# Performance work log

Hardware: AMD Instinct MI355X
Metric: run time of the kernel (lower is better)

Reference implementation:

```python
import jax, jax.numpy as jnp
import numpy as np

GRID = 10
C_IN = 4          # input_dim // (grid*grid) = 400 // 100
HID = 128         # lstm hidden_dim
NV = 6            # num_vehicles
PH = 10           # pred_horizon
BN_EPS = 1e-5


def setup_inputs() -> dict:
    key = jax.random.key(0)
    ks = jax.random.split(key, 20)
    def n(k, shape, scale=0.05):
        return jax.random.normal(k, shape, jnp.float32) * scale
    return {
        "observations": jax.random.normal(ks[0], (1024, 32, 400), jnp.float32),
        # CNN
        "conv1_w": n(ks[1], (16, C_IN, 3, 3)), "conv1_b": n(ks[2], (16,)),
        "conv2_w": n(ks[3], (32, 16, 3, 3)), "conv2_b": n(ks[4], (32,)),
        # FCN (BatchNorm in eval mode: running stats + affine)
        "fc1_w": n(ks[5], (128, 128)), "fc1_b": n(ks[6], (128,)),
        "bn1_gamma": jnp.ones((128,), jnp.float32), "bn1_beta": jnp.zeros((128,), jnp.float32),
        "bn1_mean": jnp.zeros((128,), jnp.float32), "bn1_var": jnp.ones((128,), jnp.float32),
        "fc2_w": n(ks[7], (64, 128)), "fc2_b": n(ks[8], (64,)),
        "bn2_gamma": jnp.ones((64,), jnp.float32), "bn2_beta": jnp.zeros((64,), jnp.float32),
        "bn2_mean": jnp.zeros((64,), jnp.float32), "bn2_var": jnp.ones((64,), jnp.float32),
        # encoder LSTM (torch gate order i,f,g,o; b = b_ih + b_hh fused)
        "enc_w_ih": n(ks[9], (4 * HID, 64)), "enc_w_hh": n(ks[10], (4 * HID, HID)),
        "enc_b": n(ks[11], (4 * HID,)),
        # decoder LSTM
        "dec_w_ih": n(ks[12], (4 * HID, HID)), "dec_w_hh": n(ks[13], (4 * HID, HID)),
        "dec_b": n(ks[14], (4 * HID,)),
        # output head
        "out_w": n(ks[15], (2 * NV, HID)), "out_b": n(ks[16], (2 * NV,)),
    }


def _conv(x, w, b):
    y = jax.lax.conv_general_dilated(x, w, (1, 1), "SAME",
                                     dimension_numbers=("NCHW", "OIHW", "NCHW"))
    return y + b[None, :, None, None]


def _maxpool2(x):
    # MaxPool2d(2,2) with floor (drops odd trailing row/col) == VALID
    return jax.lax.reduce_window(x, -jnp.inf, jax.lax.max, (1, 1, 2, 2), (1, 1, 2, 2), "VALID")


def _bn(x, g, b, m, v):
    return (x - m) * jax.lax.rsqrt(v + BN_EPS) * g + b


def _lstm_cell(x, h, c, w_ih, w_hh, b):
    gates = x @ w_ih.T + h @ w_hh.T + b
    i, f, g, o = jnp.split(gates, 4, axis=-1)
    c_new = jax.nn.sigmoid(f) * c + jax.nn.sigmoid(i) * jnp.tanh(g)
    h_new = jax.nn.sigmoid(o) * jnp.tanh(c_new)
    return h_new, c_new


def reference(observations, conv1_w, conv1_b, conv2_w, conv2_b,
              fc1_w, fc1_b, bn1_gamma, bn1_beta, bn1_mean, bn1_var,
              fc2_w, fc2_b, bn2_gamma, bn2_beta, bn2_mean, bn2_var,
              enc_w_ih, enc_w_hh, enc_b, dec_w_ih, dec_w_hh, dec_b,
              out_w, out_b):
    B, T, D = observations.shape
    # ---- fuse the per-frame Python loop: batch all B*T frames at once ----
    x = observations.reshape(B * T, C_IN, GRID, GRID)
    x = _maxpool2(jax.nn.relu(_conv(x, conv1_w, conv1_b)))   # [BT,16,5,5]
    x = _maxpool2(jax.nn.relu(_conv(x, conv2_w, conv2_b)))   # [BT,32,2,2]
    x = x.reshape(B * T, -1)                                 # [BT,128]
    x = jax.nn.relu(_bn(x @ fc1_w.T + fc1_b, bn1_gamma, bn1_beta, bn1_mean, bn1_var))
    x = jax.nn.relu(_bn(x @ fc2_w.T + fc2_b, bn2_gamma, bn2_beta, bn2_mean, bn2_var))
    feats = x.reshape(B, T, 64)

    # ---- encoder LSTM ----
    h0 = jnp.zeros((B, HID), feats.dtype)
    c0 = jnp.zeros((B, HID), feats.dtype)
    def enc_step(carry, xt):
        h, c = carry
        h, c = _lstm_cell(xt, h, c, enc_w_ih, enc_w_hh, enc_b)
        return (h, c), h
    (h_n, c_n), hs = jax.lax.scan(enc_step, (h0, c0), jnp.swapaxes(feats, 0, 1))
    dec_x = hs[-1]  # encoder_output[:, -1]

    def dec_step(carry, _):
        x_in, h, c = carry
        h, c = _lstm_cell(x_in, h, c, dec_w_ih, dec_w_hh, dec_b)
        pred = h @ out_w.T + out_b
        return (h, h, c), pred
    _, preds = jax.lax.scan(dec_step, (dec_x, h_n, c_n), None, length=PH)
    return jnp.swapaxes(preds, 0, 1)  # [B, PH, 2*NV]
```

## Files before the change

### kernel.cpp

```cpp
#include <hip/hip_runtime.h>
#include <hip/hip_bf16.h>
#include <hip/hip_fp16.h>

constexpr int GT = 32768;
constexpr int TSEQ = 32;

typedef _Float16 h2 __attribute__((ext_vector_type(2)));

#if defined(__has_builtin)
#if __has_builtin(__builtin_amdgcn_fdot2)
#define FDOT2(a, b, c) __builtin_amdgcn_fdot2((a), (b), (c), false)
#endif
#endif
#ifndef FDOT2
#define FDOT2(a, b, c) fmaf((float)(a).x, (float)(b).x, fmaf((float)(a).y, (float)(b).y, (c)))
#endif

__device__ __forceinline__ h2 pack2(float a, float b) {
  h2 v; v.x = (_Float16)a; v.y = (_Float16)b; return v;
}

constexpr size_t OBS_T  = 0;
constexpr size_t POOL1H = 13107200;
constexpr size_t POOL2H = 0;
constexpr size_t Y1H    = 2097152;
constexpr size_t FEATSH = 19660800;
constexpr size_t GX     = 0;
constexpr size_t WB     = 26214400;
constexpr size_t W_C1   = WB + 0;
constexpr size_t W_C2H  = WB + 576;
constexpr size_t W_F1H  = WB + 2880;
constexpr size_t B_F1   = WB + 11072;
constexpr size_t W_F2H  = WB + 11200;
constexpr size_t B_F2   = WB + 15296;
constexpr size_t W_ENCXH= WB + 15360;
constexpr size_t W_ENCHH= WB + 31744;
constexpr size_t B_ENC  = WB + 64512;
constexpr size_t W_DECH = WB + 65024;
constexpr size_t B_DEC  = WB + 97792;

__device__ __forceinline__ float sigf(float x)  { return 1.f / (1.f + __expf(-x)); }
__device__ __forceinline__ float tanhfast(float x) { return 1.f - 2.f / (__expf(2.f * x) + 1.f); }

__global__ __launch_bounds__(256) void k_setup(
    const float* __restrict__ c1w, const float* __restrict__ c2w,
    const float* __restrict__ f1w, const float* __restrict__ f1b,
    const float* __restrict__ g1, const float* __restrict__ be1,
    const float* __restrict__ m1, const float* __restrict__ v1,
    const float* __restrict__ f2w, const float* __restrict__ f2b,
    const float* __restrict__ g2, const float* __restrict__ be2,
    const float* __restrict__ m2, const float* __restrict__ v2,
    const float* __restrict__ ewih, const float* __restrict__ ewhh, const float* __restrict__ eb,
    const float* __restrict__ dwih, const float* __restrict__ dwhh, const float* __restrict__ db,
    float* __restrict__ ws) {
  h2* wsh = (h2*)ws;
  long i = (long)blockIdx.x * 256 + threadIdx.x;
  if (i < 576)  { int c = i & 15, r = i >> 4; ws[W_C1 + i] = c1w[c * 36 + r]; return; }
  i -= 576;
  if (i < 2304) { int co = i & 31, q = i >> 5; int ci2 = q / 9, t9 = q % 9;
    wsh[W_C2H + i] = pack2(c2w[co * 144 + (2 * ci2) * 9 + t9],
                           c2w[co * 144 + (2 * ci2 + 1) * 9 + t9]); return; }
  i -= 2304;
  if (i < 8192) { int j = i & 127, q = i >> 7; int co2 = q >> 2, pos = q & 3;
    float s = g1[j] * rsqrtf(v1[j] + 1e-5f);
    wsh[W_F1H + i] = pack2(f1w[j * 128 + 8 * co2 + pos] * s,
                           f1w[j * 128 + 8 * co2 + 4 + pos] * s); return; }
  i -= 8192;
  if (i < 128) { int j = i; float s = g1[j] * rsqrtf(v1[j] + 1e-5f);
    ws[B_F1 + i] = (f1b[j] - m1[j]) * s + be1[j]; return; }
  i -= 128;
  if (i < 4096) { int j = i & 63, k2 = i >> 6;
    float s = g2[j] * rsqrtf(v2[j] + 1e-5f);
    wsh[W_F2H + i] = pack2(f2w[j * 128 + 2 * k2] * s,
                           f2w[j * 128 + 2 * k2 + 1] * s); return; }
  i -= 4096;
  if (i < 64) { int j = i; float s = g2[j] * rsqrtf(v2[j] + 1e-5f);
    ws[B_F2 + i] = (f2b[j] - m2[j]) * s + be2[j]; return; }
  i -= 64;
  if (i < 16384) { int r = i & 511, k2 = i >> 9;
    int u = r >> 2, gt = r & 3, jr = gt * 128 + u;
    wsh[W_ENCXH + i] = pack2(ewih[jr * 64 + 2 * k2], ewih[jr * 64 + 2 * k2 + 1]); return; }
  i -= 16384;
  if (i < 32768) { int r = i & 511, k2 = i >> 9;
    int u = r >> 2, gt = r & 3, jr = gt * 128 + u;
    wsh[W_ENCHH + i] = pack2(ewhh[jr * 128 + 2 * k2], ewhh[jr * 128 + 2 * k2 + 1]); return; }
  i -= 32768;
  if (i < 512) { int u = i >> 2, gt = i & 3; ws[B_ENC + i] = eb[gt * 128 + u]; return; }
  i -= 512;
  if (i < 32768) { int r = i & 511, k2 = i >> 9;
    int u = r >> 2, gt = r & 3, jr = gt * 128 + u;
    wsh[W_DECH + i] = pack2(dwih[jr * 128 + 2 * k2] + dwhh[jr * 128 + 2 * k2],
                            dwih[jr * 128 + 2 * k2 + 1] + dwhh[jr * 128 + 2 * k2 + 1]); return; }
  i -= 32768;
  if (i < 512) { int u = i >> 2, gt = i & 3; ws[B_DEC + i] = db[gt * 128 + u]; return; }
}

__global__ __launch_bounds__(256) void k_transpose(const float* __restrict__ obs,
                                                   float* __restrict__ obsT) {
  __shared__ float tile[64][65];
  int tp0 = blockIdx.x * 64;
  int b0  = blockIdx.y * 64;
  int q     = threadIdx.x & 15;
  int rbase = threadIdx.x >> 4;
  #pragma unroll
  for (int rr = 0; rr < 4; ++rr) {
    int row = rbase + rr * 16;
    const float4 v = *(const float4*)(obs + (size_t)(b0 + row) * 12800 + tp0 + q * 4);
    tile[row][q * 4 + 0] = v.x;
    tile[row][q * 4 + 1] = v.y;
    tile[row][q * 4 + 2] = v.z;
    tile[row][q * 4 + 3] = v.w;
  }
  __syncthreads();
  int lane = threadIdx.x & 63;
  int grp  = threadIdx.x >> 6;
  for (int cc = 0; cc < 16; ++cc) {
    int col = grp * 16 + cc;
    int tp = tp0 + col;
    int t = tp / 400, p = tp % 400;
    obsT[(size_t)p * GT + t * 1024 + b0 + lane] = tile[lane][col];
  }
}

__global__ __launch_bounds__(256) void k_conv1(const float* __restrict__ obsT,
                                               const float* __restrict__ wT,
                                               const float* __restrict__ bias,
                                               h2* __restrict__ pool1h) {
  int g = blockIdx.x * 256 + threadIdx.x;
  int pos = blockIdx.y;
  int py = pos / 5, px = pos % 5;
  float acc[4][16];
  #pragma unroll
  for (int s = 0; s < 4; ++s)
    #pragma unroll
    for (int c = 0; c < 16; ++c) acc[s][c] = 0.f;

  #pragma unroll 1
  for (int ci = 0; ci < 4; ++ci) {
    float p[16];
    #pragma unroll
    for (int r = 0; r < 4; ++r) {
      int iy = 2 * py + r - 1;
      #pragma unroll
      for (int cx = 0; cx < 4; ++cx) {
        int ix = 2 * px + cx - 1;
        bool ok = ((unsigned)iy < 10u) && ((unsigned)ix < 10u);
        p[r * 4 + cx] = ok ? obsT[(size_t)(ci * 100 + iy * 10 + ix) * GT + g] : 0.f;
      }
    }
    #pragma unroll
    for (int t9 = 0; t9 < 9; ++t9) {
      int ky = t9 / 3, kx = t9 % 3;
      const float* w = wT + ((ci * 9 + t9) << 4);
      float wv[16];
      #pragma unroll
      for (int c = 0; c < 16; ++c) wv[c] = w[c];
      #pragma unroll
      for (int dy = 0; dy < 2; ++dy)
        #pragma unroll
        for (int dx = 0; dx < 2; ++dx) {
          float xv = p[(dy + ky) * 4 + (dx + kx)];
          #pragma unroll
          for (int c = 0; c < 16; ++c)
            acc[dy * 2 + dx][c] = fmaf(wv[c], xv, acc[dy * 2 + dx][c]);
        }
    }
  }
  float m[16];
  #pragma unroll
  for (int c = 0; c < 16; ++c) {
    float v = fmaxf(fmaxf(acc[0][c], acc[1][c]), fmaxf(acc[2][c], acc[3][c]));
    m[c] = fmaxf(v + bias[c], 0.f);
  }
  #pragma unroll
  for (int c2 = 0; c2 < 8; ++c2)
    pool1h[(size_t)(c2 * 25 + pos) * GT + g] = pack2(m[2 * c2], m[2 * c2 + 1]);
}

__global__ __launch_bounds__(256) void k_conv2h(const h2* __restrict__ pool1h,
                                                const h2* __restrict__ wch,
                                                const float* __restrict__ bias,
                                                h2* __restrict__ pool2h) {
  int g = blockIdx.x * 256 + threadIdx.x;
  int pos = blockIdx.y & 3;
  int h = blockIdx.y >> 2;
  int py = pos >> 1, px = pos & 1;
  float acc[4][8];
  #pragma unroll
  for (int s = 0; s < 4; ++s)
    #pragma unroll
    for (int c = 0; c < 8; ++c) acc[s][c] = 0.f;
  const h2 hz = pack2(0.f, 0.f);

  #pragma unroll 1
  for (int ci2 = 0; ci2 < 8; ++ci2) {
    h2 p[16];
    #pragma unroll
    for (int r = 0; r < 4; ++r) {
      int iy = 2 * py + r - 1;
      #pragma unroll
      for (int cx = 0; cx < 4; ++cx) {
        int ix = 2 * px + cx - 1;
        bool ok = ((unsigned)iy < 5u) && ((unsigned)ix < 5u);
        p[r * 4 + cx] = ok ? pool1h[(size_t)(ci2 * 25 + iy * 5 + ix) * GT + g] : hz;
      }
    }
    #pragma unroll
    for (int t9 = 0; t9 < 9; ++t9) {
      int ky = t9 / 3, kx = t9 % 3;
      const h2* w = wch + (ci2 * 9 + t9) * 32 + h * 8;
      h2 wv[8];
      #pragma unroll
      for (int c = 0; c < 8; ++c) wv[c] = w[c];
      #pragma unroll
      for (int dy = 0; dy < 2; ++dy)
        #pragma unroll
        for (int dx = 0; dx < 2; ++dx) {
          h2 xv = p[(dy + ky) * 4 + (dx + kx)];
          #pragma unroll
          for (int c = 0; c < 8; ++c)
            acc[dy * 2 + dx][c] = FDOT2(xv, wv[c], acc[dy * 2 + dx][c]);
        }
    }
  }
  float m[8];
  #pragma unroll
  for (int c = 0; c < 8; ++c) {
    float v = fmaxf(fmaxf(acc[0][c], acc[1][c]), fmaxf(acc[2][c], acc[3][c]));
    m[c] = fmaxf(v + bias[h * 8 + c], 0.f);
  }
  #pragma unroll
  for (int c2 = 0; c2 < 4; ++c2) {
    int q = (h * 4 + c2) * 4 + pos;
    pool2h[(size_t)q * GT + g] = pack2(m[2 * c2], m[2 * c2 + 1]);
  }
}

__global__ __launch_bounds__(256) void k_fc16h(const h2* __restrict__ x,
                                               const h2* __restrict__ WT,
                                               const float* __restrict__ bf,
                                               h2* __restrict__ y, int K2, int J) {
  int g = blockIdx.x * 256 + threadIdx.x;
  int j0 = blockIdx.y * 16;
  float acc[16];
  #pragma unroll
  for (int c = 0; c < 16; ++c) acc[c] = 0.f;
  for (int k2 = 0; k2 < K2; ++k2) {
    h2 xv = x[(size_t)k2 * GT + g];
    const h2* w = WT + (size_t)k2 * J + j0;
    #pragma unroll
    for (int c = 0; c < 16; ++c) acc[c] = FDOT2(xv, w[c], acc[c]);
  }
  #pragma unroll
  for (int c2 = 0; c2 < 8; ++c2) {
    float a = fmaxf(acc[2 * c2] + bf[j0 + 2 * c2], 0.f);
    float b = fmaxf(acc[2 * c2 + 1] + bf[j0 + 2 * c2 + 1], 0.f);
    y[(size_t)(j0 / 2 + c2) * GT + g] = pack2(a, b);
  }
}

__global__ __launch_bounds__(256) void k_xgatesh(const h2* __restrict__ featsh,
                                                 const h2* __restrict__ wxh,
                                                 const float* __restrict__ br,
                                                 float* __restrict__ gx) {
  int t  = blockIdx.x >> 2;
  int bq = blockIdx.x & 3;
  int b  = bq * 256 + threadIdx.x;
  int r0 = blockIdx.y * 32;
  float acc[32];
  #pragma unroll
  for (int i = 0; i < 32; ++i) acc[i] = br[r0 + i];
  const h2* xcol = featsh + (size_t)t * 1024 + b;
  for (int k2 = 0; k2 < 32; ++k2) {
    h2 xv = xcol[(size_t)k2 * GT];
    const h2* w = wxh + k2 * 512 + r0;
    #pragma unroll
    for (int i = 0; i < 32; ++i) acc[i] = FDOT2(xv, w[i], acc[i]);
  }
  float* gxs = gx + (size_t)t * 524288 + (size_t)b * 512 + r0;
  #pragma unroll
  for (int i = 0; i < 32; ++i) gxs[i] = acc[i];
}

__global__ __launch_bounds__(512, 2) void k_seq6(
    const float* __restrict__ gx,
    const h2* __restrict__ WENCH, const h2* __restrict__ WDECH,
    const float* __restrict__ bdec,
    const float* __restrict__ ow, const float* __restrict__ ob,
    float* __restrict__ out) {
  const int tid = threadIdx.x;
  const int kg  = tid & 7;
  const int g   = tid >> 3;
  const int r0  = g * 8;
  const int blo = kg & 3;
  const int bown = blockIdx.x * 4 + blo;

  __shared__ h2 hbufh[2][4 * 68];
  __shared__ h2 owl2[12 * 68];

  for (int i = tid; i < 2 * 4 * 68; i += 512) hbufh[0][i] = pack2(0.f, 0.f);
  for (int i = tid; i < 768; i += 512) {
    int o = i >> 6, k2 = i & 63;
    owl2[o * 68 + k2] = pack2(ow[o * 128 + 2 * k2], ow[o * 128 + 2 * k2 + 1]);
  }
  const float obv = (tid < 48) ? ob[tid >> 2] : 0.f;

  h2 wreg[64];
  #pragma unroll
  for (int p = 0; p < 8; ++p) {
    const h2* wp = WENCH + (size_t)(kg * 8 + p) * 512 + r0;
    *(uint4*)&wreg[p * 8]     = *(const uint4*)wp;
    *(uint4*)&wreg[p * 8 + 4] = *(const uint4*)(wp + 4);
  }

  float c0 = 0.f, c1 = 0.f;
  const int rdofs = kg * 8;
  const int wrofs = blo * 68 + g;
  __syncthreads();

  int cur = 0;

  for (int t = 0; t < TSEQ; ++t) {
    const float* gb0 = gx + (size_t)t * 524288 + (size_t)bown * 512 + r0;
    const float4 ga = *(const float4*)gb0;
    const float4 gb = *(const float4*)(gb0 + 4);

    float acc[4][8];
    #pragma unroll
    for (int bl = 0; bl < 4; ++bl)
      #pragma unroll
      for (int r = 0; r < 8; ++r) acc[bl][r] = 0.f;

    const h2* hc = &hbufh[cur][0];
    #pragma unroll
    for (int bl = 0; bl < 4; ++bl) {
      h2 hv[8];
      *(uint4*)&hv[0] = *(const uint4*)&hc[bl * 68 + rdofs];
      *(uint4*)&hv[4] = *(const uint4*)&hc[bl * 68 + rdofs + 4];
      #pragma unroll
      for (int p = 0; p < 8; ++p) {
        #pragma unroll
        for (int r = 0; r < 8; ++r)
          acc[bl][r] = FDOT2(hv[p], wreg[p * 8 + r], acc[bl][r]);
      }
    }
    float D[8];
    #pragma unroll
    for (int r = 0; r < 8; ++r) {
      float a0 = acc[0][r] + __shfl_xor(acc[0][r], 1, 64);
      float a1 = acc[1][r] + __shfl_xor(acc[1][r], 1, 64);
      float a2 = acc[2][r] + __shfl_xor(acc[2][r], 1, 64);
      float a3 = acc[3][r] + __shfl_xor(acc[3][r], 1, 64);
      float sL = (kg & 1) ? a1 : a0;
      float sH = (kg & 1) ? a3 : a2;
      float tL = sL + __shfl_xor(sL, 2, 64);
      float tH = sH + __shfl_xor(sH, 2, 64);
      float s  = (kg & 2) ? tH : tL;
      s += __shfl_xor(s, 4, 64);
      D[r] = s;
    }
    const float gi0 = D[0] + ga.x, gf0 = D[1] + ga.y, gg0 = D[2] + ga.z, go0 = D[3] + ga.w;
    const float gi1 = D[4] + gb.x, gf1 = D[5] + gb.y, gg1 = D[6] + gb.z, go1 = D[7] + gb.w;
    c0 = sigf(gf0) * c0 + sigf(gi0) * tanhfast(gg0);
    c1 = sigf(gf1) * c1 + sigf(gi1) * tanhfast(gg1);
    const float hn0 = sigf(go0) * tanhfast(c0);
    const float hn1 = sigf(go1) * tanhfast(c1);
    if (kg < 4) hbufh[cur ^ 1][wrofs] = pack2(hn0, hn1);
    __syncthreads();
    cur ^= 1;
  }

  #pragma unroll
  for (int p = 0; p < 8; ++p) {
    const h2* wp = WDECH + (size_t)(kg * 8 + p) * 512 + r0;
    *(uint4*)&wreg[p * 8]     = *(const uint4*)wp;
    *(uint4*)&wreg[p * 8 + 4] = *(const uint4*)(wp + 4);
  }
  const float4 bda = *(const float4*)(bdec + r0);
  const float4 bdb = *(const float4*)(bdec + r0 + 4);

  for (int t = 0; t < 10; ++t) {
    float acc[4][8];
    #pragma unroll
    for (int bl = 0; bl < 4; ++bl)
      #pragma unroll
      for (int r = 0; r < 8; ++r) acc[bl][r] = 0.f;

    const h2* hc = &hbufh[cur][0];
    #pragma unroll
    for (int bl = 0; bl < 4; ++bl) {
      h2 hv[8];
      *(uint4*)&hv[0] = *(const uint4*)&hc[bl * 68 + rdofs];
      *(uint4*)&hv[4] = *(const uint4*)&hc[bl * 68 + rdofs + 4];
      #pragma unroll
      for (int p = 0; p < 8; ++p) {
        #pragma unroll
        for (int r = 0; r < 8; ++r)
          acc[bl][r] = FDOT2(hv[p], wreg[p * 8 + r], acc[bl][r]);
      }
    }
    float D[8];
    #pragma unroll
    for (int r = 0; r < 8; ++r) {
      float a0 = acc[0][r] + __shfl_xor(acc[0][r], 1, 64);
      float a1 = acc[1][r] + __shfl_xor(acc[1][r], 1, 64);
      float a2 = acc[2][r] + __shfl_xor(acc[2][r], 1, 64);
      float a3 = acc[3][r] + __shfl_xor(acc[3][r], 1, 64);
      float sL = (kg & 1) ? a1 : a0;
      float sH = (kg & 1) ? a3 : a2;
      float tL = sL + __shfl_xor(sL, 2, 64);
      float tH = sH + __shfl_xor(sH, 2, 64);
      float s  = (kg & 2) ? tH : tL;
      s += __shfl_xor(s, 4, 64);
      D[r] = s;
    }
    const float gi0 = D[0] + bda.x, gf0 = D[1] + bda.y, gg0 = D[2] + bda.z, go0 = D[3] + bda.w;
    const float gi1 = D[4] + bdb.x, gf1 = D[5] + bdb.y, gg1 = D[6] + bdb.z, go1 = D[7] + bdb.w;
    c0 = sigf(gf0) * c0 + sigf(gi0) * tanhfast(gg0);
    c1 = sigf(gf1) * c1 + sigf(gi1) * tanhfast(gg1);
    const float hn0 = sigf(go0) * tanhfast(c0);
    const float hn1 = sigf(go1) * tanhfast(c1);
    if (kg < 4) hbufh[cur ^ 1][wrofs] = pack2(hn0, hn1);
    __syncthreads();
    cur ^= 1;
    if (tid < 48) {
      const int o  = tid >> 2;
      const int bh = tid & 3;
      const h2* hh = &hbufh[cur][bh * 68];
      const h2* wo = &owl2[o * 68];
      float oacc = obv;
      #pragma unroll
      for (int k2 = 0; k2 < 64; ++k2) oacc = FDOT2(hh[k2], wo[k2], oacc);
      out[(blockIdx.x * 4 + bh) * 120 + t * 12 + o] = oacc;
    }
  }
}

extern "C" void kernel_launch(void* const* d_in, const int* in_sizes, int n_in,
                              void* d_out, int out_size, void* d_ws, size_t ws_size,
                              hipStream_t stream) {
  const float* obs  = (const float*)d_in[0];
  const float* c1w  = (const float*)d_in[1];
  const float* c1b  = (const float*)d_in[2];
  const float* c2w  = (const float*)d_in[3];
  const float* c2b  = (const float*)d_in[4];
  const float* f1w  = (const float*)d_in[5];
  const float* f1b  = (const float*)d_in[6];
  const float* g1   = (const float*)d_in[7];
  const float* be1  = (const float*)d_in[8];
  const float* m1   = (const float*)d_in[9];
  const float* v1   = (const float*)d_in[10];
  const float* f2w  = (const float*)d_in[11];
  const float* f2b  = (const float*)d_in[12];
  const float* g2   = (const float*)d_in[13];
  const float* be2  = (const float*)d_in[14];
  const float* m2   = (const float*)d_in[15];
  const float* v2   = (const float*)d_in[16];
  const float* ewih = (const float*)d_in[17];
  const float* ewhh = (const float*)d_in[18];
  const float* eb   = (const float*)d_in[19];
  const float* dwih = (const float*)d_in[20];
  const float* dwhh = (const float*)d_in[21];
  const float* db   = (const float*)d_in[22];
  const float* ow   = (const float*)d_in[23];
  const float* ob   = (const float*)d_in[24];
  float* ws  = (float*)d_ws;
  h2*    wsh = (h2*)d_ws;
  float* out = (float*)d_out;

  k_setup<<<384, 256, 0, stream>>>(c1w, c2w, f1w, f1b, g1, be1, m1, v1,
                                   f2w, f2b, g2, be2, m2, v2,
                                   ewih, ewhh, eb, dwih, dwhh, db, ws);
  k_transpose<<<dim3(200, 16), 256, 0, stream>>>(obs, ws + OBS_T);
  k_conv1<<<dim3(128, 25), 256, 0, stream>>>(ws + OBS_T, ws + W_C1, c1b, wsh + POOL1H);
  k_conv2h<<<dim3(128, 16), 256, 0, stream>>>(wsh + POOL1H, wsh + W_C2H, c2b, wsh + POOL2H);
  k_fc16h<<<dim3(128, 8), 256, 0, stream>>>(wsh + POOL2H, wsh + W_F1H, ws + B_F1,
                                            wsh + Y1H, 64, 128);
  k_fc16h<<<dim3(128, 4), 256, 0, stream>>>(wsh + Y1H, wsh + W_F2H, ws + B_F2,
                                            wsh + FEATSH, 64, 64);
  k_xgatesh<<<dim3(128, 16), 256, 0, stream>>>(wsh + FEATSH, wsh + W_ENCXH, ws + B_ENC,
                                               ws + GX);
  k_seq6<<<256, 512, 0, stream>>>(ws + GX, wsh + W_ENCHH, wsh + W_DECH,
                                  ws + B_DEC, ow, ob, out);
}
```

Before: 408.7 us.

## Stage recurrent LSTM weights in shared memory and split K two ways per batch row

The sequential LSTM kernel previously kept a 64-element slice of the recurrent weights in registers per thread, with an 8-way K split that needed a three-level shuffle reduction. It now copies the full 128x512 fp16 recurrent weight matrix into two 64 KB shared arrays. Each thread owns one batch row and half of K, so only one shuffle is needed to reduce. This frees registers and cuts the cross-lane reduction, but every step now reads weights from LDS, and 128 KB of shared memory per block may limit how many blocks fit on a CU. A barrier is added after reloading the decoder weights.

```diff
diff --git a/kernel.cpp b/kernel.cpp
--- a/kernel.cpp
+++ b/kernel.cpp
@@ -282,40 +282,41 @@
   for (int i = 0; i < 32; ++i) gxs[i] = acc[i];
 }
 
-__global__ __launch_bounds__(512, 2) void k_seq6(
+__global__ __launch_bounds__(512, 2) void k_seq8(
     const float* __restrict__ gx,
     const h2* __restrict__ WENCH, const h2* __restrict__ WDECH,
     const float* __restrict__ bdec,
     const float* __restrict__ ow, const float* __restrict__ ob,
     float* __restrict__ out) {
   const int tid = threadIdx.x;
-  const int kg  = tid & 7;
+  const int bl  = tid & 3;
+  const int kg  = (tid >> 2) & 1;
   const int g   = tid >> 3;
   const int r0  = g * 8;
-  const int blo = kg & 3;
-  const int bown = blockIdx.x * 4 + blo;
-
+  const int bown = blockIdx.x * 4 + bl;
+
+  __shared__ h2 wA[16384];
+  __shared__ h2 wB[16384];
   __shared__ h2 hbufh[2][4 * 68];
   __shared__ h2 owl2[12 * 68];
 
-  for (int i = tid; i < 2 * 4 * 68; i += 512) hbufh[0][i] = pack2(0.f, 0.f);
+  for (int i = tid; i < 2 * 4 * 68; i += 512) ((h2*)hbufh)[i] = pack2(0.f, 0.f);
   for (int i = tid; i < 768; i += 512) {
     int o = i >> 6, k2 = i & 63;
     owl2[o * 68 + k2] = pack2(ow[o * 128 + 2 * k2], ow[o * 128 + 2 * k2 + 1]);
   }
   const float obv = (tid < 48) ? ob[tid >> 2] : 0.f;
 
-  h2 wreg[64];
-  #pragma unroll
-  for (int p = 0; p < 8; ++p) {
-    const h2* wp = WENCH + (size_t)(kg * 8 + p) * 512 + r0;
-    *(uint4*)&wreg[p * 8]     = *(const uint4*)wp;
-    *(uint4*)&wreg[p * 8 + 4] = *(const uint4*)(wp + 4);
+  for (int c = tid; c < 4096; c += 512) {
+    int p = c >> 7, kgc = (c >> 6) & 1, gc = c & 63;
+    const uint4* gp = (const uint4*)(WENCH + (size_t)(kgc * 32 + p) * 512 + gc * 8);
+    *(uint4*)&wA[(size_t)c * 4] = gp[0];
+    *(uint4*)&wB[(size_t)c * 4] = gp[1];
   }
 
   float c0 = 0.f, c1 = 0.f;
-  const int rdofs = kg * 8;
-  const int wrofs = blo * 68 + g;
+  const h2* wAp = &wA[(kg * 64 + g) * 4];
+  const h2* wBp = &wB[(kg * 64 + g) * 4];
   __syncthreads();
 
   int cur = 0;
@@ -325,102 +326,93 @@
     const float4 ga = *(const float4*)gb0;
     const float4 gb = *(const float4*)(gb0 + 4);
 
-    float acc[4][8];
-    #pragma unroll
-    for (int bl = 0; bl < 4; ++bl)
-      #pragma unroll
-      for (int r = 0; r < 8; ++r) acc[bl][r] = 0.f;
-
-    const h2* hc = &hbufh[cur][0];
-    #pragma unroll
-    for (int bl = 0; bl < 4; ++bl) {
-      h2 hv[8];
-      *(uint4*)&hv[0] = *(const uint4*)&hc[bl * 68 + rdofs];
-      *(uint4*)&hv[4] = *(const uint4*)&hc[bl * 68 + rdofs + 4];
-      #pragma unroll
-      for (int p = 0; p < 8; ++p) {
-        #pragma unroll
-        for (int r = 0; r < 8; ++r)
-          acc[bl][r] = FDOT2(hv[p], wreg[p * 8 + r], acc[bl][r]);
+    float acc[8];
+    #pragma unroll
+    for (int r = 0; r < 8; ++r) acc[r] = 0.f;
+
+    const h2* hp = &hbufh[cur][bl * 68 + kg * 32];
+    #pragma unroll
+    for (int pc = 0; pc < 8; ++pc) {
+      h2 hh[4];
+      *(uint4*)hh = *(const uint4*)&hp[pc * 4];
+      #pragma unroll
+      for (int j = 0; j < 4; ++j) {
+        const int p = pc * 4 + j;
+        h2 wa[4], wb[4];
+        *(uint4*)wa = *(const uint4*)&wAp[p * 512];
+        *(uint4*)wb = *(const uint4*)&wBp[p * 512];
+        acc[0] = FDOT2(hh[j], wa[0], acc[0]);
+        acc[1] = FDOT2(hh[j], wa[1], acc[1]);
+        acc[2] = FDOT2(hh[j], wa[2], acc[2]);
+        acc[3] = FDOT2(hh[j], wa[3], acc[3]);
+        acc[4] = FDOT2(hh[j], wb[0], acc[4]);
+        acc[5] = FDOT2(hh[j], wb[1], acc[5]);
+        acc[6] = FDOT2(hh[j], wb[2], acc[6]);
+        acc[7] = FDOT2(hh[j], wb[3], acc[7]);
       }
     }
     float D[8];
     #pragma unroll
-    for (int r = 0; r < 8; ++r) {
-      float a0 = acc[0][r] + __shfl_xor(acc[0][r], 1, 64);
-      float a1 = acc[1][r] + __shfl_xor(acc[1][r], 1, 64);
-      float a2 = acc[2][r] + __shfl_xor(acc[2][r], 1, 64);
-      float a3 = acc[3][r] + __shfl_xor(acc[3][r], 1, 64);
-      float sL = (kg & 1) ? a1 : a0;
-      float sH = (kg & 1) ? a3 : a2;
-      float tL = sL + __shfl_xor(sL, 2, 64);
-      float tH = sH + __shfl_xor(sH, 2, 64);
-      float s  = (kg & 2) ? tH : tL;
-      s += __shfl_xor(s, 4, 64);
-      D[r] = s;
-    }
+    for (int r = 0; r < 8; ++r) D[r] = acc[r] + __shfl_xor(acc[r], 4, 64);
+
     const float gi0 = D[0] + ga.x, gf0 = D[1] + ga.y, gg0 = D[2] + ga.z, go0 = D[3] + ga.w;
     const float gi1 = D[4] + gb.x, gf1 = D[5] + gb.y, gg1 = D[6] + gb.z, go1 = D[7] + gb.w;
     c0 = sigf(gf0) * c0 + sigf(gi0) * tanhfast(gg0);
     c1 = sigf(gf1) * c1 + sigf(gi1) * tanhfast(gg1);
     const float hn0 = sigf(go0) * tanhfast(c0);
     const float hn1 = sigf(go1) * tanhfast(c1);
-    if (kg < 4) hbufh[cur ^ 1][wrofs] = pack2(hn0, hn1);
+    if (kg == 0) hbufh[cur ^ 1][bl * 68 + g] = pack2(hn0, hn1);
     __syncthreads();
     cur ^= 1;
   }
 
-  #pragma unroll
-  for (int p = 0; p < 8; ++p) {
-    const h2* wp = WDECH + (size_t)(kg * 8 + p) * 512 + r0;
-    *(uint4*)&wreg[p * 8]     = *(const uint4*)wp;
-    *(uint4*)&wreg[p * 8 + 4] = *(const uint4*)(wp + 4);
+  for (int c = tid; c < 4096; c += 512) {
+    int p = c >> 7, kgc = (c >> 6) & 1, gc = c & 63;
+    const uint4* gp = (const uint4*)(WDECH + (size_t)(kgc * 32 + p) * 512 + gc * 8);
+    *(uint4*)&wA[(size_t)c * 4] = gp[0];
+    *(uint4*)&wB[(size_t)c * 4] = gp[1];
   }
   const float4 bda = *(const float4*)(bdec + r0);
   const float4 bdb = *(const float4*)(bdec + r0 + 4);
+  __syncthreads();
 
   for (int t = 0; t < 10; ++t) {
-    float acc[4][8];
-    #pragma unroll
-    for (int bl = 0; bl < 4; ++bl)
-      #pragma unroll
-      for (int r = 0; r < 8; ++r) acc[bl][r] = 0.f;
-
-    const h2* hc = &hbufh[cur][0];
-    #pragma unroll
-    for (int bl = 0; bl < 4; ++bl) {
-      h2 hv[8];
-      *(uint4*)&hv[0] = *(const uint4*)&hc[bl * 68 + rdofs];
-      *(uint4*)&hv[4] = *(const uint4*)&hc[bl * 68 + rdofs + 4];
-      #pragma unroll
-      for (int p = 0; p < 8; ++p) {
-        #pragma unroll
-        for (int r = 0; r < 8; ++r)
-          acc[bl][r] = FDOT2(hv[p], wreg[p * 8 + r], acc[bl][r]);
+    float acc[8];
+    #pragma unroll
+    for (int r = 0; r < 8; ++r) acc[r] = 0.f;
+
+    const h2* hp = &hbufh[cur][bl * 68 + kg * 32];
+    #pragma unroll
+    for (int pc = 0; pc < 8; ++pc) {
+      h2 hh[4];
+      *(uint4*)hh = *(const uint4*)&hp[pc * 4];
+      #pragma unroll
+      for (int j = 0; j < 4; ++j) {
+        const int p = pc * 4 + j;
+        h2 wa[4], wb[4];
+        *(uint4*)wa = *(const uint4*)&wAp[p * 512];
+        *(uint4*)wb = *(const uint4*)&wBp[p * 512];
+        acc[0] = FDOT2(hh[j], wa[0], acc[0]);
+        acc[1] = FDOT2(hh[j], wa[1], acc[1]);
+        acc[2] = FDOT2(hh[j], wa[2], acc[2]);
+        acc[3] = FDOT2(hh[j], wa[3], acc[3]);
+        acc[4] = FDOT2(hh[j], wb[0], acc[4]);
+        acc[5] = FDOT2(hh[j], wb[1], acc[5]);
+        acc[6] = FDOT2(hh[j], wb[2], acc[6]);
+        acc[7] = FDOT2(hh[j], wb[3], acc[7]);
       }
     }
     float D[8];
     #pragma unroll
-    for (int r = 0; r < 8; ++r) {
-      float a0 = acc[0][r] + __shfl_xor(acc[0][r], 1, 64);
-      float a1 = acc[1][r] + __shfl_xor(acc[1][r], 1, 64);
-      float a2 = acc[2][r] + __shfl_xor(acc[2][r], 1, 64);
-      float a3 = acc[3][r] + __shfl_xor(acc[3][r], 1, 64);
-      float sL = (kg & 1) ? a1 : a0;
-      float sH = (kg & 1) ? a3 : a2;
-      float tL = sL + __shfl_xor(sL, 2, 64);
-      float tH = sH + __shfl_xor(sH, 2, 64);
-      float s  = (kg & 2) ? tH : tL;
-      s += __shfl_xor(s, 4, 64);
-      D[r] = s;
-    }
+    for (int r = 0; r < 8; ++r) D[r] = acc[r] + __shfl_xor(acc[r], 4, 64);
+
     const float gi0 = D[0] + bda.x, gf0 = D[1] + bda.y, gg0 = D[2] + bda.z, go0 = D[3] + bda.w;
     const float gi1 = D[4] + bdb.x, gf1 = D[5] + bdb.y, gg1 = D[6] + bdb.z, go1 = D[7] + bdb.w;
     c0 = sigf(gf0) * c0 + sigf(gi0) * tanhfast(gg0);
     c1 = sigf(gf1) * c1 + sigf(gi1) * tanhfast(gg1);
     const float hn0 = sigf(go0) * tanhfast(c0);
     const float hn1 = sigf(go1) * tanhfast(c1);
-    if (kg < 4) hbufh[cur ^ 1][wrofs] = pack2(hn0, hn1);
+    if (kg == 0) hbufh[cur ^ 1][bl * 68 + g] = pack2(hn0, hn1);
     __syncthreads();
     cur ^= 1;
     if (tid < 48) {
@@ -480,6 +472,6 @@
                                             wsh + FEATSH, 64, 64);
   k_xgatesh<<<dim3(128, 16), 256, 0, stream>>>(wsh + FEATSH, wsh + W_ENCXH, ws + B_ENC,
                                                ws + GX);
-  k_seq6<<<256, 512, 0, stream>>>(ws + GX, wsh + W_ENCHH, wsh + W_DECH,
+  k_seq8<<<256, 512, 0, stream>>>(ws + GX, wsh + W_ENCHH, wsh + W_DECH,
                                   ws + B_DEC, ow, ob, out);
 }
```

Measured after the change: 388.9 us. -4.8%, faster.
